# Optimization experiments

Measured on AMD Instinct MI355X. Metric: run time of the kernel, lower is better.

## Reference

```python
import jax, jax.numpy as jnp
import numpy as np

B, N = 2, 8192
D_POINTS, D_MODEL, K = 64, 128, 16


def _lin(key, fi, fo):
    return jax.random.normal(key, (fi, fo), jnp.float32) / np.sqrt(fi)


def setup_inputs() -> dict:
    key = jax.random.key(0)
    ks = jax.random.split(key, 16)
    return {
        "xyz": jax.random.normal(ks[0], (B, N, 3), jnp.float32),
        "normals": jax.random.normal(ks[1], (B, N, 3), jnp.float32),
        "features": jax.random.normal(ks[2], (B, N, D_POINTS), jnp.float32),
        "fc1_w": _lin(ks[3], D_POINTS, D_MODEL), "fc1_b": jnp.zeros((D_MODEL,), jnp.float32),
        "fc2_w": _lin(ks[4], D_MODEL, D_POINTS), "fc2_b": jnp.zeros((D_POINTS,), jnp.float32),
        "gamma_w1": _lin(ks[5], D_MODEL, D_MODEL), "gamma_b1": jnp.zeros((D_MODEL,), jnp.float32),
        "gamma_w2": _lin(ks[6], D_MODEL, D_MODEL), "gamma_b2": jnp.zeros((D_MODEL,), jnp.float32),
        "delta_w1": _lin(ks[7], 3, D_MODEL), "delta_b1": jnp.zeros((D_MODEL,), jnp.float32),
        "delta_w2": _lin(ks[8], D_MODEL, D_MODEL), "delta_b2": jnp.zeros((D_MODEL,), jnp.float32),
        "wq": _lin(ks[9], D_MODEL, D_MODEL),
        "wk": _lin(ks[10], D_MODEL, D_MODEL),
        "wv": _lin(ks[11], D_MODEL, D_MODEL),
    }


def _gather(points, idx):
    # points: (b, n, c), idx: (b, n, k) -> (b, n, k, c)
    b, n, c = points.shape
    k = idx.shape[-1]
    flat = jnp.take_along_axis(points, idx.reshape(b, n * k, 1), axis=1)
    return flat.reshape(b, n, k, c)


def reference(xyz, normals, features, fc1_w, fc1_b, fc2_w, fc2_b,
              gamma_w1, gamma_b1, gamma_w2, gamma_b2,
              delta_w1, delta_b1, delta_w2, delta_b2, wq, wk, wv):
    # pairwise squared distances (b, n, n)
    sq = jnp.sum(xyz * xyz, axis=-1)
    dists = sq[:, :, None] + sq[:, None, :] - 2.0 * jnp.einsum('bnd,bmd->bnm', xyz, xyz)
    _, knn_idx = jax.lax.top_k(-dists, K)  # k smallest distances (includes self)

    knn_xyz = _gather(xyz, knn_idx)                      # (b, n, k, 3)
    x = features @ fc1_w + fc1_b                         # (b, n, d_model)
    q = x @ wq                                           # (b, n, d_model)
    k_nbr = _gather(x @ wk, knn_idx)                     # (b, n, k, d_model)
    v_nbr = _gather(x @ wv, knn_idx)                     # (b, n, k, d_model)

    # positional encoding: fc_delta(rel_pos), ends with ReLU
    rel = xyz[:, :, None, :] - knn_xyz                   # (b, n, k, 3)
    pos_enc = jax.nn.relu(jax.nn.relu(rel @ delta_w1 + delta_b1) @ delta_w2 + delta_b2)

    # vector attention logits: fc_gamma(q - k + pos_enc)
    h = q[:, :, None, :] - k_nbr + pos_enc
    logits = jax.nn.relu(h @ gamma_w1 + gamma_b1) @ gamma_w2 + gamma_b2
    attn = jax.nn.softmax(logits / np.sqrt(D_MODEL), axis=-2)  # softmax over neighbors

    res = jnp.einsum('bnkf,bnkf->bnf', attn, v_nbr + pos_enc)
    res = res @ fc2_w + fc2_b + features
    return res, attn
```

## Files before the change

kernel.cpp:

```cpp
#include <hip/hip_runtime.h>
#include <cstdint>

typedef unsigned long long ull;
typedef __bf16 bf16x8 __attribute__((ext_vector_type(8)));
typedef float f32x4 __attribute__((ext_vector_type(4)));

#define NPTS 8192
#define NB 2
#define KNN 16
#define DM 128
#define PADK 136

__device__ __forceinline__ float sq3f(float x, float y, float z) {
    return __fadd_rn(__fadd_rn(__fmul_rn(x, x), __fmul_rn(y, y)), __fmul_rn(z, z));
}
__device__ __forceinline__ float dot3f(float ax, float ay, float az, float bx, float by, float bz) {
    return __fadd_rn(__fadd_rn(__fmul_rn(ax, bx), __fmul_rn(ay, by)), __fmul_rn(az, bz));
}
__device__ __forceinline__ unsigned ford(float f) {
    unsigned u = __float_as_uint(f);
    return (u & 0x80000000u) ? ~u : (u | 0x80000000u);
}

__global__ __launch_bounds__(256) void knn_kernel(const float* __restrict__ xyz,
                                                  int* __restrict__ idx_out) {
    __shared__ float4 xs4[1024];
    const int t = threadIdx.x;
    const int wv = t >> 6, lane = t & 63;
    const int q_id = blockIdx.x * 4 + wv;
    const int b = q_id >> 13;
    const int i = q_id & (NPTS - 1);
    const float* xb = xyz + (size_t)b * NPTS * 3;
    const float qx = xb[3 * i + 0], qy = xb[3 * i + 1], qz = xb[3 * i + 2];
    const float sqi = sq3f(qx, qy, qz);

    unsigned list_hi = 0xffffffffu, list_lo = 0xffffffffu;
    unsigned thr_hi = 0xffffffffu, thr_lo = 0xffffffffu;

    for (int ch = 0; ch < 8; ++ch) {
        __syncthreads();
#pragma unroll
        for (int e = 0; e < 4; e++) {
            int p = t + e * 256;
            int g = ch * 1024 + p;
            float x = xb[3 * g + 0], y = xb[3 * g + 1], z = xb[3 * g + 2];
            xs4[p] = make_float4(x, y, z, sq3f(x, y, z));
        }
        __syncthreads();
#pragma unroll 4
        for (int m = 0; m < 16; m++) {
            int jl = m * 64 + lane;
            float4 P = xs4[jl];
            float d = __fsub_rn(__fadd_rn(sqi, P.w),
                                __fmul_rn(2.0f, dot3f(qx, qy, qz, P.x, P.y, P.z)));
            unsigned du = ford(d);
            unsigned jme = (unsigned)(ch * 1024 + jl);
            bool trig = (du < thr_hi) || (du == thr_hi && jme < thr_lo);
            ull ballot = __ballot(trig);
            if (ballot == 0ull) continue;
            const unsigned jbase = (unsigned)(ch * 1024 + m * 64);
            do {
                int l = (int)__builtin_ctzll(ballot);
                ballot &= ballot - 1;
                unsigned ck_hi = (unsigned)__builtin_amdgcn_readlane((int)du, l);
                unsigned ck_lo = jbase + (unsigned)l;
                unsigned ph = __shfl_up(list_hi, 1);
                unsigned pl = __shfl_up(list_lo, 1);
                bool ck_lt_list = (ck_hi < list_hi) || (ck_hi == list_hi && ck_lo < list_lo);
                bool ck_ge_prev = (lane == 0) || (ck_hi > ph) || (ck_hi == ph && ck_lo >= pl);
                unsigned nh = ck_ge_prev ? ck_hi : ph;
                unsigned nl = ck_ge_prev ? ck_lo : pl;
                list_hi = ck_lt_list ? nh : list_hi;
                list_lo = ck_lt_list ? nl : list_lo;
            } while (ballot);
            thr_hi = (unsigned)__builtin_amdgcn_readlane((int)list_hi, 15);
            thr_lo = (unsigned)__builtin_amdgcn_readlane((int)list_lo, 15);
        }
    }
    if (lane < 16)
        idx_out[q_id * 16 + lane] = (int)list_lo;
}

__global__ __launch_bounds__(256) void wprep_kernel(const float* __restrict__ d2,
                                                    const float* __restrict__ g1,
                                                    const float* __restrict__ g2,
                                                    __bf16* __restrict__ d2t,
                                                    __bf16* __restrict__ g1t,
                                                    __bf16* __restrict__ g2t) {
    const float* src = (blockIdx.x == 0) ? d2 : ((blockIdx.x == 1) ? g1 : g2);
    __bf16* dst = (blockIdx.x == 0) ? d2t : ((blockIdx.x == 1) ? g1t : g2t);
#pragma unroll
    for (int e = 0; e < 64; e++) {
        int id = threadIdx.x + e * 256;
        int k = id >> 7, n = id & 127;
        dst[n * 128 + k] = (__bf16)src[id];
    }
}

__global__ __launch_bounds__(256, 1) void gemm_x_kernel(const float* __restrict__ feats,
                                                        const float* __restrict__ w,
                                                        const float* __restrict__ bias,
                                                        float* __restrict__ xout) {
    __shared__ float At[64 * 65];
    __shared__ __align__(16) float Wt[64 * 128];
    const int t = threadIdx.x;
    const int base = blockIdx.x * 64;
#pragma unroll
    for (int e = 0; e < 16; e++) {
        int id = t + e * 256;
        int r = id >> 6, c = id & 63;
        At[c * 65 + r] = feats[(size_t)(base + r) * 64 + c];
    }
#pragma unroll
    for (int e = 0; e < 32; e++) { int id = t + e * 256; Wt[id] = w[id]; }
    __syncthreads();
    const int r0 = (t >> 4) * 4;
    const int c0 = (t & 15) * 8;
    float acc[4][8];
#pragma unroll
    for (int i = 0; i < 4; i++)
#pragma unroll
        for (int j = 0; j < 8; j++) acc[i][j] = bias[c0 + j];
#pragma unroll 4
    for (int kk = 0; kk < 64; ++kk) {
        float a0 = At[kk * 65 + r0 + 0];
        float a1 = At[kk * 65 + r0 + 1];
        float a2 = At[kk * 65 + r0 + 2];
        float a3 = At[kk * 65 + r0 + 3];
        const float4 w0 = *(const float4*)&Wt[kk * 128 + c0];
        const float4 w1 = *(const float4*)&Wt[kk * 128 + c0 + 4];
        float wj[8] = {w0.x, w0.y, w0.z, w0.w, w1.x, w1.y, w1.z, w1.w};
#pragma unroll
        for (int j = 0; j < 8; j++) {
            acc[0][j] += a0 * wj[j];
            acc[1][j] += a1 * wj[j];
            acc[2][j] += a2 * wj[j];
            acc[3][j] += a3 * wj[j];
        }
    }
#pragma unroll
    for (int i = 0; i < 4; i++)
#pragma unroll
        for (int j = 0; j < 8; j++)
            xout[(size_t)(base + r0 + i) * 128 + c0 + j] = acc[i][j];
}

__global__ __launch_bounds__(256, 1) void gemm_qkv_kernel(const float* __restrict__ x,
                                                          const float* __restrict__ wq,
                                                          const float* __restrict__ wk,
                                                          const float* __restrict__ wv,
                                                          float* __restrict__ qo,
                                                          float* __restrict__ ko,
                                                          float* __restrict__ vo) {
    const float* w = (blockIdx.y == 0) ? wq : ((blockIdx.y == 1) ? wk : wv);
    float* o = (blockIdx.y == 0) ? qo : ((blockIdx.y == 1) ? ko : vo);
    __shared__ float At[128 * 65];
    __shared__ __align__(16) float Wt[128 * 128];
    const int t = threadIdx.x;
    const int base = blockIdx.x * 64;
#pragma unroll
    for (int e = 0; e < 32; e++) {
        int id = t + e * 256;
        int r = id >> 7, c = id & 127;
        At[c * 65 + r] = x[(size_t)(base + r) * 128 + c];
    }
#pragma unroll
    for (int e = 0; e < 64; e++) { int id = t + e * 256; Wt[id] = w[id]; }
    __syncthreads();
    const int r0 = (t >> 4) * 4;
    const int c0 = (t & 15) * 8;
    float acc[4][8];
#pragma unroll
    for (int i = 0; i < 4; i++)
#pragma unroll
        for (int j = 0; j < 8; j++) acc[i][j] = 0.0f;
#pragma unroll 4
    for (int kk = 0; kk < 128; ++kk) {
        float a0 = At[kk * 65 + r0 + 0];
        float a1 = At[kk * 65 + r0 + 1];
        float a2 = At[kk * 65 + r0 + 2];
        float a3 = At[kk * 65 + r0 + 3];
        const float4 w0 = *(const float4*)&Wt[kk * 128 + c0];
        const float4 w1 = *(const float4*)&Wt[kk * 128 + c0 + 4];
        float wj[8] = {w0.x, w0.y, w0.z, w0.w, w1.x, w1.y, w1.z, w1.w};
#pragma unroll
        for (int j = 0; j < 8; j++) {
            acc[0][j] += a0 * wj[j];
            acc[1][j] += a1 * wj[j];
            acc[2][j] += a2 * wj[j];
            acc[3][j] += a3 * wj[j];
        }
    }
#pragma unroll
    for (int i = 0; i < 4; i++)
#pragma unroll
        for (int j = 0; j < 8; j++)
            o[(size_t)(base + r0 + i) * 128 + c0 + j] = acc[i][j];
}

#define DO_GEMM(ACC0, ACC1, WPTR)                                                          \
    {                                                                                      \
        _Pragma("unroll")                                                                  \
        for (int kt = 0; kt < 4; kt++) {                                                   \
            const int ko = kt * 32 + 8 * lg;                                               \
            bf16x8 a0 = *(const bf16x8*)&Ab[(rbase + lr) * PADK + ko];                     \
            bf16x8 a1 = *(const bf16x8*)&Ab[(rbase + 16 + lr) * PADK + ko];                \
            _Pragma("unroll")                                                              \
            for (int ct = 0; ct < 8; ct++) {                                               \
                bf16x8 bv = *(const bf16x8*)&WPTR[(ct * 16 + lr) * PADK + ko];             \
                ACC0[ct] = __builtin_amdgcn_mfma_f32_16x16x32_bf16(a0, bv, ACC0[ct], 0, 0, 0); \
                ACC1[ct] = __builtin_amdgcn_mfma_f32_16x16x32_bf16(a1, bv, ACC1[ct], 0, 0, 0); \
            }                                                                              \
        }                                                                                  \
    }

#define STAGE_W(SRC)                                                                       \
    {                                                                                      \
        _Pragma("unroll")                                                                  \
        for (int e = 0; e < 8; e++) {                                                      \
            int ch = t + e * 256;                                                          \
            int r = ch >> 4, ck = ch & 15;                                                 \
            *(bf16x8*)&Wb[r * PADK + ck * 8] = *(const bf16x8*)&SRC[r * 128 + ck * 8];     \
        }                                                                                  \
    }

__global__ __launch_bounds__(256, 2) void k345_kernel(const float* __restrict__ xyz,
                                                      const int* __restrict__ idxw,
                                                      const float* __restrict__ q,
                                                      const float* __restrict__ xk,
                                                      const float* __restrict__ xv,
                                                      const float* __restrict__ d1,
                                                      const float* __restrict__ bd1,
                                                      const float* __restrict__ bd2,
                                                      const float* __restrict__ bg1,
                                                      const float* __restrict__ bg2,
                                                      const __bf16* __restrict__ d2t,
                                                      const __bf16* __restrict__ g1t,
                                                      const __bf16* __restrict__ g2t,
                                                      float* __restrict__ attn,
                                                      float* __restrict__ res_pre) {
    __shared__ __bf16 Ab[128 * PADK];
    __shared__ __bf16 Wb[128 * PADK];
    __shared__ float rels[128 * 4];
    __shared__ int jrow[128];
    __shared__ float d1s[3 * 128];
    __shared__ float bd1s[128], bd2s[128], bg1s[128], bg2s[128];

    const int t = threadIdx.x;
    const int wv = t >> 6;
    const int lane = t & 63;
    const int lr = lane & 15, lg = lane >> 4;
    const int R0 = blockIdx.x * 128;
    const int b = R0 >> 17;
    const int rbase = wv * 32;

#pragma unroll
    for (int e = 0; e < 2; e++) { int id = t + e * 256; if (id < 384) d1s[id] = d1[id]; }
    if (t < 128) {
        bd1s[t] = bd1[t]; bd2s[t] = bd2[t]; bg1s[t] = bg1[t]; bg2s[t] = bg2[t];
    } else {
        int r = t - 128;
        int j = idxw[R0 + r];
        jrow[r] = j;
        const float* pn = xyz + (size_t)((R0 + r) >> 4) * 3;
        const float* pj = xyz + (size_t)((b << 13) + j) * 3;
        rels[r * 4 + 0] = pn[0] - pj[0];
        rels[r * 4 + 1] = pn[1] - pj[1];
        rels[r * 4 + 2] = pn[2] - pj[2];
    }
    STAGE_W(d2t)
    __syncthreads();

    {
        const int c = t & 127;
        const float w0 = d1s[c], w1 = d1s[128 + c], w2 = d1s[256 + c], bb = bd1s[c];
#pragma unroll
        for (int e = 0; e < 64; e++) {
            int r = (t >> 7) + e * 2;
            float v = fmaf(rels[r * 4 + 2], w2,
                      fmaf(rels[r * 4 + 1], w1, fmaf(rels[r * 4 + 0], w0, bb)));
            Ab[r * PADK + c] = (__bf16)fmaxf(v, 0.0f);
        }
    }
    __syncthreads();

    f32x4 acc0[8], acc1[8];
#pragma unroll
    for (int ct = 0; ct < 8; ct++) {
        float bb = bd2s[ct * 16 + lr];
        acc0[ct] = (f32x4){bb, bb, bb, bb};
        acc1[ct] = acc0[ct];
    }
    DO_GEMM(acc0, acc1, Wb)
    f32x4 pos0[8], pos1[8];
#pragma unroll
    for (int ct = 0; ct < 8; ct++) {
#pragma unroll
        for (int e = 0; e < 4; e++) {
            pos0[ct][e] = fmaxf(acc0[ct][e], 0.0f);
            pos1[ct][e] = fmaxf(acc1[ct][e], 0.0f);
        }
    }

#pragma unroll
    for (int rt = 0; rt < 2; rt++) {
        const int rloc = rbase + rt * 16 + 4 * lg;
        const size_t qbase = (size_t)((R0 + rloc) >> 4) * 128;
        const int j0 = jrow[rloc + 0], j1 = jrow[rloc + 1];
        const int j2 = jrow[rloc + 2], j3 = jrow[rloc + 3];
        const size_t kb0 = (size_t)((b << 13) + j0) * 128;
        const size_t kb1 = (size_t)((b << 13) + j1) * 128;
        const size_t kb2 = (size_t)((b << 13) + j2) * 128;
        const size_t kb3 = (size_t)((b << 13) + j3) * 128;
        f32x4* posR = rt ? pos1 : pos0;
#pragma unroll
        for (int ct = 0; ct < 8; ct++) {
            const int c = ct * 16 + lr;
            const float qv = q[qbase + c];
            f32x4 p = posR[ct];
            Ab[(rloc + 0) * PADK + c] = (__bf16)(p[0] + qv - xk[kb0 + c]);
            Ab[(rloc + 1) * PADK + c] = (__bf16)(p[1] + qv - xk[kb1 + c]);
            Ab[(rloc + 2) * PADK + c] = (__bf16)(p[2] + qv - xk[kb2 + c]);
            Ab[(rloc + 3) * PADK + c] = (__bf16)(p[3] + qv - xk[kb3 + c]);
        }
    }
    __syncthreads();
    STAGE_W(g1t)
    __syncthreads();

#pragma unroll
    for (int ct = 0; ct < 8; ct++) {
        float bb = bg1s[ct * 16 + lr];
        acc0[ct] = (f32x4){bb, bb, bb, bb};
        acc1[ct] = acc0[ct];
    }
    DO_GEMM(acc0, acc1, Wb)
#pragma unroll
    for (int rt = 0; rt < 2; rt++) {
        const int rloc = rbase + rt * 16 + 4 * lg;
        f32x4* accR = rt ? acc1 : acc0;
#pragma unroll
        for (int ct = 0; ct < 8; ct++) {
            const int c = ct * 16 + lr;
            f32x4 p = accR[ct];
            Ab[(rloc + 0) * PADK + c] = (__bf16)fmaxf(p[0], 0.0f);
            Ab[(rloc + 1) * PADK + c] = (__bf16)fmaxf(p[1], 0.0f);
            Ab[(rloc + 2) * PADK + c] = (__bf16)fmaxf(p[2], 0.0f);
            Ab[(rloc + 3) * PADK + c] = (__bf16)fmaxf(p[3], 0.0f);
        }
    }
    __syncthreads();
    STAGE_W(g2t)
    __syncthreads();

#pragma unroll
    for (int ct = 0; ct < 8; ct++) {
        float bb = bg2s[ct * 16 + lr];
        acc0[ct] = (f32x4){bb, bb, bb, bb};
        acc1[ct] = acc0[ct];
    }
    DO_GEMM(acc0, acc1, Wb)
    const float scale = 0.08838834764831845f;
#pragma unroll
    for (int rt = 0; rt < 2; rt++) {
        const int rloc = rbase + rt * 16 + 4 * lg;
        const int j0 = jrow[rloc + 0], j1 = jrow[rloc + 1];
        const int j2 = jrow[rloc + 2], j3 = jrow[rloc + 3];
        const size_t vb0 = (size_t)((b << 13) + j0) * 128;
        const size_t vb1 = (size_t)((b << 13) + j1) * 128;
        const size_t vb2 = (size_t)((b << 13) + j2) * 128;
        const size_t vb3 = (size_t)((b << 13) + j3) * 128;
        f32x4* accR = rt ? acc1 : acc0;
        f32x4* posR = rt ? pos1 : pos0;
#pragma unroll
        for (int ct = 0; ct < 8; ct++) {
            const int c = ct * 16 + lr;
            f32x4 p = accR[ct];
            float l0 = p[0] * scale, l1 = p[1] * scale, l2 = p[2] * scale, l3 = p[3] * scale;
            float m = fmaxf(fmaxf(l0, l1), fmaxf(l2, l3));
            m = fmaxf(m, __shfl_xor(m, 16));
            m = fmaxf(m, __shfl_xor(m, 32));
            float e0 = __expf(l0 - m), e1 = __expf(l1 - m);
            float e2 = __expf(l2 - m), e3 = __expf(l3 - m);
            float s = (e0 + e1) + (e2 + e3);
            s += __shfl_xor(s, 16);
            s += __shfl_xor(s, 32);
            float inv = 1.0f / s;
            float a0 = e0 * inv, a1 = e1 * inv, a2 = e2 * inv, a3 = e3 * inv;
            size_t ob = (size_t)(R0 + rloc) * 128 + c;
            attn[ob + 0 * 128] = a0;
            attn[ob + 1 * 128] = a1;
            attn[ob + 2 * 128] = a2;
            attn[ob + 3 * 128] = a3;
            f32x4 pp = posR[ct];
            float r = a0 * (xv[vb0 + c] + pp[0])
                    + a1 * (xv[vb1 + c] + pp[1])
                    + a2 * (xv[vb2 + c] + pp[2])
                    + a3 * (xv[vb3 + c] + pp[3]);
            r += __shfl_xor(r, 16);
            r += __shfl_xor(r, 32);
            if (lg == 0)
                res_pre[(size_t)((R0 >> 4) + wv * 2 + rt) * 128 + c] = r;
        }
    }
}

__global__ __launch_bounds__(256, 1) void k6_kernel(const float* __restrict__ res_pre,
                                                    const float* __restrict__ w,
                                                    const float* __restrict__ bias,
                                                    const float* __restrict__ feats,
                                                    float* __restrict__ res_out) {
    __shared__ float At[128 * 65];
    __shared__ __align__(16) float Wt[128 * 64];
    const int t = threadIdx.x;
    const int base = blockIdx.x * 64;
#pragma unroll
    for (int e = 0; e < 32; e++) {
        int id = t + e * 256;
        int r = id >> 7, c = id & 127;
        At[c * 65 + r] = res_pre[(size_t)(base + r) * 128 + c];
    }
#pragma unroll
    for (int e = 0; e < 32; e++) { int id = t + e * 256; Wt[id] = w[id]; }
    __syncthreads();
    const int r0 = (t >> 4) * 4;
    const int c0 = (t & 15) * 4;
    float acc[4][4];
#pragma unroll
    for (int i = 0; i < 4; i++)
#pragma unroll
        for (int j = 0; j < 4; j++) acc[i][j] = bias[c0 + j];
#pragma unroll 4
    for (int kk = 0; kk < 128; ++kk) {
        float a0 = At[kk * 65 + r0 + 0];
        float a1 = At[kk * 65 + r0 + 1];
        float a2 = At[kk * 65 + r0 + 2];
        float a3 = At[kk * 65 + r0 + 3];
        const float4 w0 = *(const float4*)&Wt[kk * 64 + c0];
        float wj[4] = {w0.x, w0.y, w0.z, w0.w};
#pragma unroll
        for (int j = 0; j < 4; j++) {
            acc[0][j] += a0 * wj[j];
            acc[1][j] += a1 * wj[j];
            acc[2][j] += a2 * wj[j];
            acc[3][j] += a3 * wj[j];
        }
    }
#pragma unroll
    for (int i = 0; i < 4; i++)
#pragma unroll
        for (int j = 0; j < 4; j++)
            res_out[(size_t)(base + r0 + i) * 64 + c0 + j] =
                acc[i][j] + feats[(size_t)(base + r0 + i) * 64 + c0 + j];
}

extern "C" void kernel_launch(void* const* d_in, const int* in_sizes, int n_in,
                              void* d_out, int out_size, void* d_ws, size_t ws_size,
                              hipStream_t stream) {
    (void)in_sizes; (void)n_in; (void)out_size; (void)ws_size;
    const float* xyz   = (const float*)d_in[0];
    const float* feats = (const float*)d_in[2];
    const float* fc1_w = (const float*)d_in[3];
    const float* fc1_b = (const float*)d_in[4];
    const float* fc2_w = (const float*)d_in[5];
    const float* fc2_b = (const float*)d_in[6];
    const float* g1    = (const float*)d_in[7];
    const float* bg1   = (const float*)d_in[8];
    const float* g2    = (const float*)d_in[9];
    const float* bg2   = (const float*)d_in[10];
    const float* d1    = (const float*)d_in[11];
    const float* bd1   = (const float*)d_in[12];
    const float* d2    = (const float*)d_in[13];
    const float* bd2   = (const float*)d_in[14];
    const float* wq    = (const float*)d_in[15];
    const float* wk    = (const float*)d_in[16];
    const float* wv    = (const float*)d_in[17];

    int* idxw   = (int*)d_ws;
    float* xbuf = (float*)((char*)d_ws + (1 << 20));
    float* qbuf = xbuf + 2097152;
    float* kbuf = qbuf + 2097152;
    float* vbuf = kbuf + 2097152;
    float* rpre = vbuf + 2097152;
    __bf16* d2t = (__bf16*)(rpre + 2097152);
    __bf16* g1t = d2t + 16384;
    __bf16* g2t = g1t + 16384;

    float* res_out = (float*)d_out;
    float* attn    = res_out + 1048576;

    wprep_kernel<<<3, 256, 0, stream>>>(d2, g1, g2, d2t, g1t, g2t);
    knn_kernel<<<4096, 256, 0, stream>>>(xyz, idxw);
    gemm_x_kernel<<<256, 256, 0, stream>>>(feats, fc1_w, fc1_b, xbuf);
    gemm_qkv_kernel<<<dim3(256, 3), 256, 0, stream>>>(xbuf, wq, wk, wv, qbuf, kbuf, vbuf);
    k345_kernel<<<2048, 256, 0, stream>>>(xyz, idxw, qbuf, kbuf, vbuf, d1, bd1, bd2, bg1, bg2,
                                          d2t, g1t, g2t, attn, rpre);
    k6_kernel<<<256, 256, 0, stream>>>(rpre, fc2_w, fc2_b, feats, res_out);
}
```

Baseline: 288.9 us.

## Process two candidates per lane in KNN scan with float threshold compare

The KNN scan now evaluates two candidate points per lane per iteration and does a single ballot for both. Candidates are filtered with a plain float compare against a running threshold instead of a packed (key, index) compare. The threshold is refreshed after every insertion rather than once per batch, and the chunk load uses vectorized float4 reads. This cuts per-candidate compare and ballot overhead in the dominant KNN kernel, at the cost of extra serial insertion work when both halves pass and a change in how ties are screened.

```diff
diff --git a/kernel.cpp b/kernel.cpp
--- a/kernel.cpp
+++ b/kernel.cpp
@@ -17,9 +17,12 @@
 __device__ __forceinline__ float dot3f(float ax, float ay, float az, float bx, float by, float bz) {
     return __fadd_rn(__fadd_rn(__fmul_rn(ax, bx), __fmul_rn(ay, by)), __fmul_rn(az, bz));
 }
-__device__ __forceinline__ unsigned ford(float f) {
-    unsigned u = __float_as_uint(f);
+__device__ __forceinline__ unsigned ford(unsigned u) {
     return (u & 0x80000000u) ? ~u : (u | 0x80000000u);
+}
+__device__ __forceinline__ float inv_ford(unsigned f) {
+    unsigned u = (f & 0x80000000u) ? (f ^ 0x80000000u) : ~f;
+    return __uint_as_float(u);
 }
 
 __global__ __launch_bounds__(256) void knn_kernel(const float* __restrict__ xyz,
@@ -35,46 +38,60 @@
     const float sqi = sq3f(qx, qy, qz);
 
     unsigned list_hi = 0xffffffffu, list_lo = 0xffffffffu;
-    unsigned thr_hi = 0xffffffffu, thr_lo = 0xffffffffu;
+    float thrF = __uint_as_float(0x7f800000u);
 
     for (int ch = 0; ch < 8; ++ch) {
         __syncthreads();
-#pragma unroll
-        for (int e = 0; e < 4; e++) {
-            int p = t + e * 256;
-            int g = ch * 1024 + p;
-            float x = xb[3 * g + 0], y = xb[3 * g + 1], z = xb[3 * g + 2];
-            xs4[p] = make_float4(x, y, z, sq3f(x, y, z));
+        {
+            const float* src = xb + ch * 3072 + t * 12;
+            float4 f0 = *(const float4*)(src);
+            float4 f1 = *(const float4*)(src + 4);
+            float4 f2 = *(const float4*)(src + 8);
+            xs4[t * 4 + 0] = make_float4(f0.x, f0.y, f0.z, sq3f(f0.x, f0.y, f0.z));
+            xs4[t * 4 + 1] = make_float4(f0.w, f1.x, f1.y, sq3f(f0.w, f1.x, f1.y));
+            xs4[t * 4 + 2] = make_float4(f1.z, f1.w, f2.x, sq3f(f1.z, f1.w, f2.x));
+            xs4[t * 4 + 3] = make_float4(f2.y, f2.z, f2.w, sq3f(f2.y, f2.z, f2.w));
         }
         __syncthreads();
-#pragma unroll 4
-        for (int m = 0; m < 16; m++) {
-            int jl = m * 64 + lane;
+        for (int m = 0; m < 8; m++) {
+            const int jl = m * 128 + lane;
             float4 P = xs4[jl];
-            float d = __fsub_rn(__fadd_rn(sqi, P.w),
-                                __fmul_rn(2.0f, dot3f(qx, qy, qz, P.x, P.y, P.z)));
-            unsigned du = ford(d);
-            unsigned jme = (unsigned)(ch * 1024 + jl);
-            bool trig = (du < thr_hi) || (du == thr_hi && jme < thr_lo);
-            ull ballot = __ballot(trig);
+            float4 Q = xs4[jl + 64];
+            float dA = __fsub_rn(__fadd_rn(sqi, P.w),
+                                 __fmul_rn(2.0f, dot3f(qx, qy, qz, P.x, P.y, P.z)));
+            float dB = __fsub_rn(__fadd_rn(sqi, Q.w),
+                                 __fmul_rn(2.0f, dot3f(qx, qy, qz, Q.x, Q.y, Q.z)));
+            bool ta = (dA <= thrF), tb = (dB <= thrF);
+            ull ballot = __ballot(ta || tb);
             if (ballot == 0ull) continue;
-            const unsigned jbase = (unsigned)(ch * 1024 + m * 64);
+            const unsigned jbase = (unsigned)(ch * 1024 + m * 128);
             do {
                 int l = (int)__builtin_ctzll(ballot);
                 ballot &= ballot - 1;
-                unsigned ck_hi = (unsigned)__builtin_amdgcn_readlane((int)du, l);
-                unsigned ck_lo = jbase + (unsigned)l;
-                unsigned ph = __shfl_up(list_hi, 1);
-                unsigned pl = __shfl_up(list_lo, 1);
-                bool ck_lt_list = (ck_hi < list_hi) || (ck_hi == list_hi && ck_lo < list_lo);
-                bool ck_ge_prev = (lane == 0) || (ck_hi > ph) || (ck_hi == ph && ck_lo >= pl);
-                unsigned nh = ck_ge_prev ? ck_hi : ph;
-                unsigned nl = ck_ge_prev ? ck_lo : pl;
-                list_hi = ck_lt_list ? nh : list_hi;
-                list_lo = ck_lt_list ? nl : list_lo;
+                float fA = __uint_as_float(
+                    (unsigned)__builtin_amdgcn_readlane(__float_as_int(dA), l));
+                float fB = __uint_as_float(
+                    (unsigned)__builtin_amdgcn_readlane(__float_as_int(dB), l));
+#pragma unroll
+                for (int half = 0; half < 2; half++) {
+                    float fc = half ? fB : fA;
+                    if (fc <= thrF) {
+                        unsigned ck_hi = ford(__float_as_uint(fc));
+                        unsigned ck_lo = jbase + (unsigned)l + (half ? 64u : 0u);
+                        unsigned ph = __shfl_up(list_hi, 1);
+                        unsigned pl = __shfl_up(list_lo, 1);
+                        bool lt = (ck_hi < list_hi) || (ck_hi == list_hi && ck_lo < list_lo);
+                        bool ge = (lane == 0) || (ck_hi > ph) || (ck_hi == ph && ck_lo >= pl);
+                        unsigned nh = ge ? ck_hi : ph;
+                        unsigned nl = ge ? ck_lo : pl;
+                        list_hi = lt ? nh : list_hi;
+                        list_lo = lt ? nl : list_lo;
+                        unsigned th = (unsigned)__builtin_amdgcn_readlane((int)list_hi, 15);
+                        th = (th > 0xff800000u) ? 0xff800000u : th;
+                        thrF = inv_ford(th);
+                    }
+                }
             } while (ballot);
-            thr_hi = (unsigned)__builtin_amdgcn_readlane((int)list_hi, 15);
-            thr_lo = (unsigned)__builtin_amdgcn_readlane((int)list_lo, 15);
         }
     }
     if (lane < 16)
```

New measurement: 295.1 us. +2.2%, slower.
